# Kernel tuning notes

Hardware: AMD Instinct MI355X
Metric: run time of the kernel (lower is better)

Reference implementation:

```python
import jax, jax.numpy as jnp
import numpy as np

DT = 1.0
TOL = 2e-4
MAX_FK = 0.1


def _lap(x):
    # 5-point Laplacian with periodic boundary (roll-based), x: [B,1,H,W]
    return (jnp.roll(x, 1, -1) + jnp.roll(x, -1, -1)
            + jnp.roll(x, 1, -2) + jnp.roll(x, -1, -2) - 4.0 * x)


def _gs_step(u, v, Du, Dv, F, k, dt):
    uvv = u * v * v
    u_next = u + dt * (Du * _lap(u) - uvv + F * (1.0 - u))
    v_next = v + dt * (Dv * _lap(v) + uvv - (F + k) * v)
    return u_next, v_next


def setup_inputs() -> dict:
    key = jax.random.key(0)
    k1, k2 = jax.random.split(key)
    B, H, W = 32, 512, 512
    # physically sensible Gray-Scott init: u near 1, v small
    u = 1.0 - 0.5 * jax.random.uniform(k1, (B, 1, H, W), dtype=jnp.float32)
    v = 0.25 * jax.random.uniform(k2, (B, 1, H, W), dtype=jnp.float32)
    return {
        "u": u,
        "v": v,
        "log_Du": jnp.float32(-2.0),
        "log_Dv": jnp.float32(-2.0),
        "raw_F": jnp.float32(0.0),
        "raw_k": jnp.float32(0.0),
        "max_steps": 64,
        "K": 32,
    }


def reference(u, v, log_Du, log_Dv, raw_F, raw_k, max_steps, K):
    # params_tensor()
    Du = jax.nn.softplus(log_Du)
    Dv = jax.nn.softplus(log_Dv)
    F = MAX_FK * jax.nn.sigmoid(raw_F)
    k = MAX_FK * jax.nn.sigmoid(raw_k)

    B = u.shape[0]
    converged0 = jnp.zeros((B,), dtype=bool)

    # Phase 1: simulate-until-converged (per-sample freeze), expressed as a
    # fixed-length masked scan (no data-dependent shapes). Samples that were
    # already converged at the start of a step keep their state frozen,
    # matching the index_select/scatter semantics of the torch loop.
    def steady_body(carry, _):
        u, v, conv = carry
        u_next, v_next = _gs_step(u, v, Du, Dv, F, k, DT)
        du = jnp.max(jnp.abs(u_next - u), axis=(1, 2, 3))
        dv = jnp.max(jnp.abs(v_next - v), axis=(1, 2, 3))
        newly = jnp.maximum(du, dv) < TOL
        m = conv[:, None, None, None]
        u2 = jnp.where(m, u, u_next)
        v2 = jnp.where(m, v, v_next)
        return (u2, v2, conv | newly), None

    (u, v, converged), _ = jax.lax.scan(
        steady_body, (u, v, converged0), None, length=max_steps)

    # Phase 2: K differentiable steps (trunc BPTT segment), no masking
    def bptt_body(carry, _):
        u, v = carry
        return _gs_step(u, v, Du, Dv, F, k, DT), None

    (u, v), _ = jax.lax.scan(bptt_body, (u, v), None, length=K)
    return (u, v)
```

## Files before the change

kernel.cpp:

```cpp
#include <hip/hip_runtime.h>

#define HH 512
#define WW 512
#define BB 32
#define NIMG (HH * WW)
#define NT (BB * NIMG)
#define TOLF 0.0002f
#define TR 16
#define TI (TR + 2)
#define NTB (HH / TR)

__device__ __forceinline__ void gs_math(
    const float4& cu, const float4& uu, const float4& ud, float ul, float ur,
    const float4& cv, const float4& vu, const float4& vd, float vl, float vr,
    float Du, float Dv, float F, float Fk, float4& un, float4& vn)
{
    float4 lu, lv;
    lu.x = ul   + cu.y + uu.x + ud.x - 4.f * cu.x;
    lu.y = cu.x + cu.z + uu.y + ud.y - 4.f * cu.y;
    lu.z = cu.y + cu.w + uu.z + ud.z - 4.f * cu.z;
    lu.w = cu.z + ur   + uu.w + ud.w - 4.f * cu.w;
    lv.x = vl   + cv.y + vu.x + vd.x - 4.f * cv.x;
    lv.y = cv.x + cv.z + vu.y + vd.y - 4.f * cv.y;
    lv.z = cv.y + cv.w + vu.z + vd.z - 4.f * cv.z;
    lv.w = cv.z + vr   + vu.w + vd.w - 4.f * cv.w;
    float uvv;
    uvv  = cu.x * cv.x * cv.x;
    un.x = cu.x + (Du * lu.x - uvv + F * (1.f - cu.x));
    vn.x = cv.x + (Dv * lv.x + uvv - Fk * cv.x);
    uvv  = cu.y * cv.y * cv.y;
    un.y = cu.y + (Du * lu.y - uvv + F * (1.f - cu.y));
    vn.y = cv.y + (Dv * lv.y + uvv - Fk * cv.y);
    uvv  = cu.z * cv.z * cv.z;
    un.z = cu.z + (Du * lu.z - uvv + F * (1.f - cu.z));
    vn.z = cv.z + (Dv * lv.z + uvv - Fk * cv.z);
    uvv  = cu.w * cv.w * cv.w;
    un.w = cu.w + (Du * lu.w - uvv + F * (1.f - cu.w));
    vn.w = cv.w + (Dv * lv.w + uvv - Fk * cv.w);
}

__device__ __forceinline__ void load_row(const float* __restrict__ s,
                                         int base, int baseUp, int baseDn, int c0,
                                         float4& c, float4& up, float4& dn, float& l, float& r)
{
    c  = *(const float4*)(s + base   + c0);
    up = *(const float4*)(s + baseUp + c0);
    dn = *(const float4*)(s + baseDn + c0);
    l  = s[base + ((c0 - 1) & (WW - 1))];
    r  = s[base + ((c0 + 4) & (WW - 1))];
}

__device__ __forceinline__ float dmax8(const float4& un, const float4& cu,
                                       const float4& vn, const float4& cv)
{
    return fmaxf(
        fmaxf(fmaxf(fabsf(un.x - cu.x), fabsf(un.y - cu.y)),
              fmaxf(fabsf(un.z - cu.z), fabsf(un.w - cu.w))),
        fmaxf(fmaxf(fabsf(vn.x - cv.x), fabsf(vn.y - cv.y)),
              fmaxf(fabsf(vn.z - cv.z), fabsf(vn.w - cv.w))));
}

__launch_bounds__(256, 2)
__global__ void gs_pair(const float* __restrict__ fsU, const float* __restrict__ fsV,
                        float* wsU, float* wsV, float* outU, float* outV,
                        const float* __restrict__ consts,
                        const int* __restrict__ conv, const int* __restrict__ par,
                        float* __restrict__ pmaxA, float* __restrict__ pmaxB,
                        int tpar, int steady)
{
    __shared__ float iu[TI][WW];
    __shared__ float iv[TI][WW];
    __shared__ float s1[4], s2[4];

    const int b = blockIdx.y;
    if (steady && conv[b]) return;
    const int p = par[b] ^ tpar;
    const float* __restrict__ su = p ? outU : wsU;
    const float* __restrict__ sv = p ? outV : wsV;
    float* __restrict__ dU = p ? wsU : outU;
    float* __restrict__ dV = p ? wsV : outV;
    if (fsU) { su = fsU; sv = fsV; }

    const float Du = consts[0], Dv = consts[1], F = consts[2], Fk = consts[3];

    const int t  = threadIdx.x;
    const int c0 = (t & 127) * 4;
    const int rw = t >> 7;
    const int r0 = blockIdx.x * TR;

    float dm1 = 0.f;
    #pragma unroll
    for (int i = 0; i < TI; i += 2) {
        const int li = i + rw;
        const int h  = (r0 - 1 + li) & (HH - 1);
        const int hm = (h - 1) & (HH - 1);
        const int hp = (h + 1) & (HH - 1);
        const int base   = b * NIMG + h  * WW;
        const int baseUp = b * NIMG + hm * WW;
        const int baseDn = b * NIMG + hp * WW;
        float4 cu, uu, ud, cv, vu, vd; float ul, ur, vl, vr;
        load_row(su, base, baseUp, baseDn, c0, cu, uu, ud, ul, ur);
        load_row(sv, base, baseUp, baseDn, c0, cv, vu, vd, vl, vr);
        float4 un, vn;
        gs_math(cu, uu, ud, ul, ur, cv, vu, vd, vl, vr, Du, Dv, F, Fk, un, vn);
        *(float4*)(&iu[li][c0]) = un;
        *(float4*)(&iv[li][c0]) = vn;
        if (steady) dm1 = fmaxf(dm1, dmax8(un, cu, vn, cv));
    }
    __syncthreads();

    float dm2 = 0.f;
    #pragma unroll
    for (int i = 0; i < TR; i += 2) {
        const int li = 1 + i + rw;
        const int h  = r0 + i + rw;
        float4 cu = *(const float4*)(&iu[li][c0]);
        float4 uu = *(const float4*)(&iu[li - 1][c0]);
        float4 ud = *(const float4*)(&iu[li + 1][c0]);
        const float ul = iu[li][(c0 - 1) & (WW - 1)];
        const float ur = iu[li][(c0 + 4) & (WW - 1)];
        float4 cv = *(const float4*)(&iv[li][c0]);
        float4 vu = *(const float4*)(&iv[li - 1][c0]);
        float4 vd = *(const float4*)(&iv[li + 1][c0]);
        const float vl = iv[li][(c0 - 1) & (WW - 1)];
        const float vr = iv[li][(c0 + 4) & (WW - 1)];
        float4 un, vn;
        gs_math(cu, uu, ud, ul, ur, cv, vu, vd, vl, vr, Du, Dv, F, Fk, un, vn);
        *(float4*)(dU + b * NIMG + h * WW + c0) = un;
        *(float4*)(dV + b * NIMG + h * WW + c0) = vn;
        if (steady) dm2 = fmaxf(dm2, dmax8(un, cu, vn, cv));
    }

    if (steady) {
        #pragma unroll
        for (int off = 1; off < 64; off <<= 1) {
            dm1 = fmaxf(dm1, __shfl_xor(dm1, off));
            dm2 = fmaxf(dm2, __shfl_xor(dm2, off));
        }
        const int wid = t >> 6;
        if ((t & 63) == 0) { s1[wid] = dm1; s2[wid] = dm2; }
        __syncthreads();
        if (t == 0) {
            pmaxA[b * NTB + blockIdx.x] = fmaxf(fmaxf(s1[0], s1[1]), fmaxf(s1[2], s1[3]));
            pmaxB[b * NTB + blockIdx.x] = fmaxf(fmaxf(s2[0], s2[1]), fmaxf(s2[2], s2[3]));
        }
    }
}

__launch_bounds__(256, 2)
__global__ void gs_upd(const float* __restrict__ fsU, const float* __restrict__ fsV,
                       float* wsU, float* wsV, float* outU, float* outV,
                       const float* __restrict__ consts,
                       const int* __restrict__ convO, const int* __restrict__ parO,
                       int* convN, int* parN,
                       const float* __restrict__ pmaxA, const float* __restrict__ pmaxB)
{
    __shared__ float sAB[2];
    const int b = blockIdx.y;
    const int t = threadIdx.x;
    if (convO[b]) {
        if (blockIdx.x == 0 && t == 0) { convN[b] = 1; parN[b] = parO[b]; }
        return;
    }
    if (t < 64) {
        float a = (t < NTB) ? pmaxA[b * NTB + t] : 0.f;
        float c = (t < NTB) ? pmaxB[b * NTB + t] : 0.f;
        #pragma unroll
        for (int off = 1; off < 32; off <<= 1) {
            a = fmaxf(a, __shfl_xor(a, off));
            c = fmaxf(c, __shfl_xor(c, off));
        }
        if (t == 0) { sAB[0] = a; sAB[1] = c; }
    }
    __syncthreads();
    const float d1 = sAB[0], d2 = sAB[1];
    const int pO = parO[b];
    if (blockIdx.x == 0 && t == 0) {
        parN[b]  = pO ^ 1;
        convN[b] = (d1 < TOLF) || (d2 < TOLF);
    }
    if (d1 < TOLF) {
        const float* __restrict__ su = pO ? outU : wsU;
        const float* __restrict__ sv = pO ? outV : wsV;
        float* __restrict__ dU = pO ? wsU : outU;
        float* __restrict__ dV = pO ? wsV : outV;
        if (fsU) { su = fsU; sv = fsV; }
        const float Du = consts[0], Dv = consts[1], F = consts[2], Fk = consts[3];
        const int c0 = (t & 127) * 4;
        const int rw = t >> 7;
        const int r0 = blockIdx.x * TR;
        for (int i = 0; i < TR; i += 2) {
            const int h  = r0 + i + rw;
            const int hm = (h - 1) & (HH - 1);
            const int hp = (h + 1) & (HH - 1);
            const int base   = b * NIMG + h  * WW;
            const int baseUp = b * NIMG + hm * WW;
            const int baseDn = b * NIMG + hp * WW;
            float4 cu, uu, ud, cv, vu, vd; float ul, ur, vl, vr;
            load_row(su, base, baseUp, baseDn, c0, cu, uu, ud, ul, ur);
            load_row(sv, base, baseUp, baseDn, c0, cv, vu, vd, vl, vr);
            float4 un, vn;
            gs_math(cu, uu, ud, ul, ur, cv, vu, vd, vl, vr, Du, Dv, F, Fk, un, vn);
            *(float4*)(dU + base + c0) = un;
            *(float4*)(dV + base + c0) = vn;
        }
    }
}

__global__ void gs_init(const float* lDu, const float* lDv, const float* rF, const float* rk,
                        float* consts, int* conv0, int* par0)
{
    const int t = threadIdx.x;
    if (t == 0) {
        const float a = lDu[0], c = lDv[0];
        const float Du = (a > 0.f) ? a + log1pf(expf(-a)) : log1pf(expf(a));
        const float Dv = (c > 0.f) ? c + log1pf(expf(-c)) : log1pf(expf(c));
        const float F  = 0.1f / (1.f + expf(-rF[0]));
        const float kk = 0.1f / (1.f + expf(-rk[0]));
        consts[0] = Du; consts[1] = Dv; consts[2] = F; consts[3] = F + kk;
    }
    if (t < BB) { conv0[t] = 0; par0[t] = 0; }
}

__launch_bounds__(256)
__global__ void gs_final(const float* __restrict__ wsU, const float* __restrict__ wsV,
                         float* outU, float* outV, const int* __restrict__ par)
{
    const int b = blockIdx.y;
    if (par[b] != 0) return;
    const int off = b * NIMG + (blockIdx.x * 256 + threadIdx.x) * 4;
    *(float4*)(outU + off) = *(const float4*)(wsU + off);
    *(float4*)(outV + off) = *(const float4*)(wsV + off);
}

extern "C" void kernel_launch(void* const* d_in, const int* in_sizes, int n_in,
                              void* d_out, int out_size, void* d_ws, size_t ws_size,
                              hipStream_t stream)
{
    const float* in_u = (const float*)d_in[0];
    const float* in_v = (const float*)d_in[1];
    const float* lDu  = (const float*)d_in[2];
    const float* lDv  = (const float*)d_in[3];
    const float* rF   = (const float*)d_in[4];
    const float* rk   = (const float*)d_in[5];
    const int NPAIR_STEADY = 32;
    const int NPAIR_BPTT   = 16;

    float* wsU = (float*)d_ws;
    float* wsV = wsU + NT;
    float* aux = wsV + NT;
    float* consts = aux;
    int* conv0 = (int*)(aux + 4);
    int* par0  = conv0 + BB;
    int* conv1 = par0 + BB;
    int* par1  = conv1 + BB;
    float* pmaxA = (float*)(par1 + BB);
    float* pmaxB = pmaxA + BB * NTB;

    float* outU = (float*)d_out;
    float* outV = outU + NT;

    gs_init<<<1, 64, 0, stream>>>(lDu, lDv, rF, rk, consts, conv0, par0);

    const dim3 grid(NTB, BB);
    for (int s = 0; s < NPAIR_STEADY; ++s) {
        int* cO = (s & 1) ? conv1 : conv0;
        int* pO = (s & 1) ? par1  : par0;
        int* cN = (s & 1) ? conv0 : conv1;
        int* pN = (s & 1) ? par0  : par1;
        const float* fU = (s == 0) ? in_u : nullptr;
        const float* fV = (s == 0) ? in_v : nullptr;
        gs_pair<<<grid, 256, 0, stream>>>(fU, fV, wsU, wsV, outU, outV, consts,
                                          cO, pO, pmaxA, pmaxB, 0, 1);
        gs_upd<<<grid, 256, 0, stream>>>(fU, fV, wsU, wsV, outU, outV, consts,
                                         cO, pO, cN, pN, pmaxA, pmaxB);
    }
    for (int j = 0; j < NPAIR_BPTT; ++j) {
        gs_pair<<<grid, 256, 0, stream>>>(nullptr, nullptr, wsU, wsV, outU, outV, consts,
                                          conv0, par0, pmaxA, pmaxB, j & 1, 0);
    }
    gs_final<<<dim3(NIMG / 1024, BB), 256, 0, stream>>>(wsU, wsV, outU, outV, par0);
}
```

Measured before the change: 1.595 ms.

## Fuse four Gray-Scott steps per kernel with rolling shared-memory ring pipeline

Replaces the two-step temporal-blocked kernel with a four-step kernel that streams 32-row strips through a chain of 5-row shared-memory ring buffers. Each intermediate step is computed from the previous stage's ring, and per-step max-deltas are recorded for the convergence check. The aim is to halve global memory traffic and kernel launches per simulated step. Samples that converge partway through a quad are recomputed from the quad's input by rollback kernels (rollA does two steps, rollB one), which adds launches and extra work on convergence. The strip grid is smaller (16x32 blocks) and the kernel uses more shared memory, which may lower occupancy.

```diff
diff --git a/kernel.cpp b/kernel.cpp
--- a/kernel.cpp
+++ b/kernel.cpp
@@ -6,9 +6,11 @@
 #define NIMG (HH * WW)
 #define NT (BB * NIMG)
 #define TOLF 0.0002f
-#define TR 16
-#define TI (TR + 2)
-#define NTB (HH / TR)
+#define HS 32
+#define NSTRIP (HH / HS)
+#define TRP 16
+#define TIP (TRP + 2)
+#define NTBP (HH / TRP)
 
 __device__ __forceinline__ void gs_math(
     const float4& cu, const float4& uu, const float4& ud, float ul, float ur,
@@ -39,17 +41,6 @@
     vn.w = cv.w + (Dv * lv.w + uvv - Fk * cv.w);
 }
 
-__device__ __forceinline__ void load_row(const float* __restrict__ s,
-                                         int base, int baseUp, int baseDn, int c0,
-                                         float4& c, float4& up, float4& dn, float& l, float& r)
-{
-    c  = *(const float4*)(s + base   + c0);
-    up = *(const float4*)(s + baseUp + c0);
-    dn = *(const float4*)(s + baseDn + c0);
-    l  = s[base + ((c0 - 1) & (WW - 1))];
-    r  = s[base + ((c0 + 4) & (WW - 1))];
-}
-
 __device__ __forceinline__ float dmax8(const float4& un, const float4& cu,
                                        const float4& vn, const float4& cv)
 {
@@ -60,17 +51,41 @@
               fmaxf(fabsf(vn.z - cv.z), fabsf(vn.w - cv.w))));
 }
 
-__launch_bounds__(256, 2)
-__global__ void gs_pair(const float* __restrict__ fsU, const float* __restrict__ fsV,
-                        float* wsU, float* wsV, float* outU, float* outV,
-                        const float* __restrict__ consts,
-                        const int* __restrict__ conv, const int* __restrict__ par,
-                        float* __restrict__ pmaxA, float* __restrict__ pmaxB,
-                        int tpar, int steady)
-{
-    __shared__ float iu[TI][WW];
-    __shared__ float iv[TI][WW];
-    __shared__ float s1[4], s2[4];
+__device__ __forceinline__ int s5(int r) { int m = r % 5; return m < 0 ? m + 5 : m; }
+
+__device__ __forceinline__ void produce_ring(
+    const float (* __restrict__ Su)[WW], const float (* __restrict__ Sv)[WW],
+    float (* __restrict__ Tu)[WW], float (* __restrict__ Tv)[WW],
+    int r, int c0, float Du, float Dv, float F, float Fk, float& dm, bool acc)
+{
+    const int sm = s5(r - 1), s0 = s5(r), sp = s5(r + 1);
+    const int cl = (c0 - 4) & (WW - 1), cr = (c0 + 4) & (WW - 1);
+    const float4 cu = *(const float4*)&Su[s0][c0];
+    const float4 uu = *(const float4*)&Su[sm][c0];
+    const float4 ud = *(const float4*)&Su[sp][c0];
+    const float  ul = ((const float4*)&Su[s0][cl])->w;
+    const float  ur = ((const float4*)&Su[s0][cr])->x;
+    const float4 cv = *(const float4*)&Sv[s0][c0];
+    const float4 vu = *(const float4*)&Sv[sm][c0];
+    const float4 vd = *(const float4*)&Sv[sp][c0];
+    const float  vl = ((const float4*)&Sv[s0][cl])->w;
+    const float  vr = ((const float4*)&Sv[s0][cr])->x;
+    float4 un, vn;
+    gs_math(cu, uu, ud, ul, ur, cv, vu, vd, vl, vr, Du, Dv, F, Fk, un, vn);
+    *(float4*)&Tu[s0][c0] = un;
+    *(float4*)&Tv[s0][c0] = vn;
+    if (acc) dm = fmaxf(dm, dmax8(un, cu, vn, cv));
+}
+
+__global__ __launch_bounds__(256)
+void gs_quad(const float* __restrict__ fsU, const float* __restrict__ fsV,
+             float* wsU, float* wsV, float* outU, float* outV,
+             const float* __restrict__ consts,
+             const int* __restrict__ conv, const int* __restrict__ par,
+             float* __restrict__ pmax, int tpar, int steady)
+{
+    __shared__ float Iu[5][WW], Iv[5][WW], Au[5][WW], Av[5][WW],
+                     Bu[5][WW], Bv[5][WW], Cu[5][WW], Cv[5][WW];
 
     const int b = blockIdx.y;
     if (steady && conv[b]) return;
@@ -82,15 +97,170 @@
     if (fsU) { su = fsU; sv = fsV; }
 
     const float Du = consts[0], Dv = consts[1], F = consts[2], Fk = consts[3];
-
     const int t  = threadIdx.x;
+    const int rw = t >> 7;
     const int c0 = (t & 127) * 4;
-    const int rw = t >> 7;
-    const int r0 = blockIdx.x * TR;
-
-    float dm1 = 0.f;
+    const int R0 = blockIdx.x * HS;
+    const size_t ib = (size_t)b * NIMG;
+
+    float d1 = 0.f, d2 = 0.f, d3 = 0.f, d4 = 0.f;
+
+    float4 pu, pv;
+    {   const int g = (R0 - 4 + rw) & (HH - 1);
+        pu = *(const float4*)(su + ib + (size_t)g * WW + c0);
+        pv = *(const float4*)(sv + ib + (size_t)g * WW + c0);
+    }
+
+    for (int i = 0; i < 24; ++i) {
+        const int rI = 2*i - 4  + rw;
+        const int rA = 2*i - 6  + rw;
+        const int rB = 2*i - 10 + rw;
+        const int rC = 2*i - 12 + rw;
+        const int rO = 2*i - 16 + rw;
+
+        if (rI <= HS + 3) {
+            const int s = s5(rI);
+            *(float4*)&Iu[s][c0] = pu;
+            *(float4*)&Iv[s][c0] = pv;
+        }
+        if (rB >= -2 && rB <= HS + 1)
+            produce_ring(Au, Av, Bu, Bv, rB, c0, Du, Dv, F, Fk, d2,
+                         steady && rB >= 0 && rB < HS);
+        if (rO >= 0 && rO < HS) {
+            const int sm = s5(rO - 1), s0 = s5(rO), sp = s5(rO + 1);
+            const int cl = (c0 - 4) & (WW - 1), cr = (c0 + 4) & (WW - 1);
+            const float4 cu = *(const float4*)&Cu[s0][c0];
+            const float4 uu = *(const float4*)&Cu[sm][c0];
+            const float4 ud = *(const float4*)&Cu[sp][c0];
+            const float  ul = ((const float4*)&Cu[s0][cl])->w;
+            const float  ur = ((const float4*)&Cu[s0][cr])->x;
+            const float4 cv = *(const float4*)&Cv[s0][c0];
+            const float4 vu = *(const float4*)&Cv[sm][c0];
+            const float4 vd = *(const float4*)&Cv[sp][c0];
+            const float  vl = ((const float4*)&Cv[s0][cl])->w;
+            const float  vr = ((const float4*)&Cv[s0][cr])->x;
+            float4 un, vn;
+            gs_math(cu, uu, ud, ul, ur, cv, vu, vd, vl, vr, Du, Dv, F, Fk, un, vn);
+            *(float4*)(dU + ib + (size_t)(R0 + rO) * WW + c0) = un;
+            *(float4*)(dV + ib + (size_t)(R0 + rO) * WW + c0) = vn;
+            if (steady) d4 = fmaxf(d4, dmax8(un, cu, vn, cv));
+        }
+        __syncthreads();
+
+        {   const int rn = 2*i - 2 + rw;
+            if (rn <= HS + 3) {
+                const int g = (R0 + rn) & (HH - 1);
+                pu = *(const float4*)(su + ib + (size_t)g * WW + c0);
+                pv = *(const float4*)(sv + ib + (size_t)g * WW + c0);
+            }
+        }
+
+        if (rA >= -3 && rA <= HS + 2)
+            produce_ring(Iu, Iv, Au, Av, rA, c0, Du, Dv, F, Fk, d1,
+                         steady && rA >= 0 && rA < HS);
+        if (rC >= -1 && rC <= HS)
+            produce_ring(Bu, Bv, Cu, Cv, rC, c0, Du, Dv, F, Fk, d3,
+                         steady && rC >= 0 && rC < HS);
+        __syncthreads();
+    }
+
+    if (steady) {
+        #pragma unroll
+        for (int off = 1; off < 64; off <<= 1) {
+            d1 = fmaxf(d1, __shfl_xor(d1, off));
+            d2 = fmaxf(d2, __shfl_xor(d2, off));
+            d3 = fmaxf(d3, __shfl_xor(d3, off));
+            d4 = fmaxf(d4, __shfl_xor(d4, off));
+        }
+        const int w = t >> 6;
+        if ((t & 63) == 0) {
+            Iu[0][w * 4 + 0] = d1; Iu[0][w * 4 + 1] = d2;
+            Iu[0][w * 4 + 2] = d3; Iu[0][w * 4 + 3] = d4;
+        }
+        __syncthreads();
+        if (t == 0) {
+            float m0 = 0.f, m1 = 0.f, m2 = 0.f, m3 = 0.f;
+            #pragma unroll
+            for (int w2 = 0; w2 < 4; ++w2) {
+                m0 = fmaxf(m0, Iu[0][w2 * 4 + 0]);
+                m1 = fmaxf(m1, Iu[0][w2 * 4 + 1]);
+                m2 = fmaxf(m2, Iu[0][w2 * 4 + 2]);
+                m3 = fmaxf(m3, Iu[0][w2 * 4 + 3]);
+            }
+            const int idx = b * NSTRIP + blockIdx.x;
+            pmax[0 * BB * NSTRIP + idx] = m0;
+            pmax[1 * BB * NSTRIP + idx] = m1;
+            pmax[2 * BB * NSTRIP + idx] = m2;
+            pmax[3 * BB * NSTRIP + idx] = m3;
+        }
+    }
+}
+
+__global__ void gs_upd(const int* __restrict__ convO, const int* __restrict__ parO,
+                       int* convN, int* parN, int* rbJ,
+                       const float* __restrict__ pmax)
+{
+    const int b = blockIdx.x, t = threadIdx.x;
+    if (convO[b]) { if (t == 0) { convN[b] = 1; parN[b] = parO[b]; rbJ[b] = 0; } return; }
+    float v0 = 0.f, v1 = 0.f, v2 = 0.f, v3 = 0.f;
+    if (t < NSTRIP) {
+        const int idx = b * NSTRIP + t;
+        v0 = pmax[0 * BB * NSTRIP + idx];
+        v1 = pmax[1 * BB * NSTRIP + idx];
+        v2 = pmax[2 * BB * NSTRIP + idx];
+        v3 = pmax[3 * BB * NSTRIP + idx];
+    }
     #pragma unroll
-    for (int i = 0; i < TI; i += 2) {
+    for (int off = 1; off < NSTRIP; off <<= 1) {
+        v0 = fmaxf(v0, __shfl_xor(v0, off));
+        v1 = fmaxf(v1, __shfl_xor(v1, off));
+        v2 = fmaxf(v2, __shfl_xor(v2, off));
+        v3 = fmaxf(v3, __shfl_xor(v3, off));
+    }
+    if (t == 0) {
+        int j = 0;
+        if      (v0 < TOLF) j = 1;
+        else if (v1 < TOLF) j = 2;
+        else if (v2 < TOLF) j = 3;
+        else if (v3 < TOLF) j = 4;
+        const int pO = parO[b];
+        convN[b] = (j != 0);
+        parN[b]  = (j == 3) ? pO : (pO ^ 1);
+        rbJ[b]   = (j >= 1 && j <= 3) ? j : 0;
+    }
+}
+
+__device__ __forceinline__ void load_row(const float* __restrict__ s,
+                                         int base, int baseUp, int baseDn, int c0,
+                                         float4& c, float4& up, float4& dn, float& l, float& r)
+{
+    c  = *(const float4*)(s + base   + c0);
+    up = *(const float4*)(s + baseUp + c0);
+    dn = *(const float4*)(s + baseDn + c0);
+    l  = s[base + ((c0 - 1) & (WW - 1))];
+    r  = s[base + ((c0 + 4) & (WW - 1))];
+}
+
+__global__ __launch_bounds__(256)
+void gs_rollA(const float* __restrict__ fsU, const float* __restrict__ fsV,
+              float* wsU, float* wsV, float* outU, float* outV,
+              const float* __restrict__ consts,
+              const int* __restrict__ parO, const int* __restrict__ rbJ)
+{
+    __shared__ float iu[TIP][WW];
+    __shared__ float iv[TIP][WW];
+    const int b = blockIdx.y;
+    if (rbJ[b] < 2) return;
+    const int p = parO[b];
+    const float* __restrict__ su = p ? outU : wsU;
+    const float* __restrict__ sv = p ? outV : wsV;
+    float* __restrict__ dU = p ? wsU : outU;
+    float* __restrict__ dV = p ? wsV : outV;
+    if (fsU) { su = fsU; sv = fsV; }
+    const float Du = consts[0], Dv = consts[1], F = consts[2], Fk = consts[3];
+    const int t = threadIdx.x, c0 = (t & 127) * 4, rw = t >> 7;
+    const int r0 = blockIdx.x * TRP;
+    for (int i = 0; i < TIP; i += 2) {
         const int li = i + rw;
         const int h  = (r0 - 1 + li) & (HH - 1);
         const int hm = (h - 1) & (HH - 1);
@@ -105,13 +275,9 @@
         gs_math(cu, uu, ud, ul, ur, cv, vu, vd, vl, vr, Du, Dv, F, Fk, un, vn);
         *(float4*)(&iu[li][c0]) = un;
         *(float4*)(&iv[li][c0]) = vn;
-        if (steady) dm1 = fmaxf(dm1, dmax8(un, cu, vn, cv));
     }
     __syncthreads();
-
-    float dm2 = 0.f;
-    #pragma unroll
-    for (int i = 0; i < TR; i += 2) {
+    for (int i = 0; i < TRP; i += 2) {
         const int li = 1 + i + rw;
         const int h  = r0 + i + rw;
         float4 cu = *(const float4*)(&iu[li][c0]);
@@ -128,87 +294,44 @@
         gs_math(cu, uu, ud, ul, ur, cv, vu, vd, vl, vr, Du, Dv, F, Fk, un, vn);
         *(float4*)(dU + b * NIMG + h * WW + c0) = un;
         *(float4*)(dV + b * NIMG + h * WW + c0) = vn;
-        if (steady) dm2 = fmaxf(dm2, dmax8(un, cu, vn, cv));
-    }
-
-    if (steady) {
-        #pragma unroll
-        for (int off = 1; off < 64; off <<= 1) {
-            dm1 = fmaxf(dm1, __shfl_xor(dm1, off));
-            dm2 = fmaxf(dm2, __shfl_xor(dm2, off));
-        }
-        const int wid = t >> 6;
-        if ((t & 63) == 0) { s1[wid] = dm1; s2[wid] = dm2; }
-        __syncthreads();
-        if (t == 0) {
-            pmaxA[b * NTB + blockIdx.x] = fmaxf(fmaxf(s1[0], s1[1]), fmaxf(s1[2], s1[3]));
-            pmaxB[b * NTB + blockIdx.x] = fmaxf(fmaxf(s2[0], s2[1]), fmaxf(s2[2], s2[3]));
-        }
-    }
-}
-
-__launch_bounds__(256, 2)
-__global__ void gs_upd(const float* __restrict__ fsU, const float* __restrict__ fsV,
-                       float* wsU, float* wsV, float* outU, float* outV,
-                       const float* __restrict__ consts,
-                       const int* __restrict__ convO, const int* __restrict__ parO,
-                       int* convN, int* parN,
-                       const float* __restrict__ pmaxA, const float* __restrict__ pmaxB)
-{
-    __shared__ float sAB[2];
+    }
+}
+
+__global__ __launch_bounds__(256)
+void gs_rollB(const float* __restrict__ fsU, const float* __restrict__ fsV,
+              float* wsU, float* wsV, float* outU, float* outV,
+              const float* __restrict__ consts,
+              const int* __restrict__ parO, const int* __restrict__ rbJ)
+{
     const int b = blockIdx.y;
-    const int t = threadIdx.x;
-    if (convO[b]) {
-        if (blockIdx.x == 0 && t == 0) { convN[b] = 1; parN[b] = parO[b]; }
-        return;
-    }
-    if (t < 64) {
-        float a = (t < NTB) ? pmaxA[b * NTB + t] : 0.f;
-        float c = (t < NTB) ? pmaxB[b * NTB + t] : 0.f;
-        #pragma unroll
-        for (int off = 1; off < 32; off <<= 1) {
-            a = fmaxf(a, __shfl_xor(a, off));
-            c = fmaxf(c, __shfl_xor(c, off));
-        }
-        if (t == 0) { sAB[0] = a; sAB[1] = c; }
-    }
-    __syncthreads();
-    const float d1 = sAB[0], d2 = sAB[1];
-    const int pO = parO[b];
-    if (blockIdx.x == 0 && t == 0) {
-        parN[b]  = pO ^ 1;
-        convN[b] = (d1 < TOLF) || (d2 < TOLF);
-    }
-    if (d1 < TOLF) {
-        const float* __restrict__ su = pO ? outU : wsU;
-        const float* __restrict__ sv = pO ? outV : wsV;
-        float* __restrict__ dU = pO ? wsU : outU;
-        float* __restrict__ dV = pO ? wsV : outV;
-        if (fsU) { su = fsU; sv = fsV; }
-        const float Du = consts[0], Dv = consts[1], F = consts[2], Fk = consts[3];
-        const int c0 = (t & 127) * 4;
-        const int rw = t >> 7;
-        const int r0 = blockIdx.x * TR;
-        for (int i = 0; i < TR; i += 2) {
-            const int h  = r0 + i + rw;
-            const int hm = (h - 1) & (HH - 1);
-            const int hp = (h + 1) & (HH - 1);
-            const int base   = b * NIMG + h  * WW;
-            const int baseUp = b * NIMG + hm * WW;
-            const int baseDn = b * NIMG + hp * WW;
-            float4 cu, uu, ud, cv, vu, vd; float ul, ur, vl, vr;
-            load_row(su, base, baseUp, baseDn, c0, cu, uu, ud, ul, ur);
-            load_row(sv, base, baseUp, baseDn, c0, cv, vu, vd, vl, vr);
-            float4 un, vn;
-            gs_math(cu, uu, ud, ul, ur, cv, vu, vd, vl, vr, Du, Dv, F, Fk, un, vn);
-            *(float4*)(dU + base + c0) = un;
-            *(float4*)(dV + base + c0) = vn;
-        }
-    }
+    const int j = rbJ[b];
+    if (j != 1 && j != 3) return;
+    const int q = parO[b] ^ (j == 3 ? 1 : 0);
+    const float* __restrict__ su = q ? outU : wsU;
+    const float* __restrict__ sv = q ? outV : wsV;
+    float* __restrict__ dU = q ? wsU : outU;
+    float* __restrict__ dV = q ? wsV : outV;
+    if (j == 1 && fsU) { su = fsU; sv = fsV; }
+    const float Du = consts[0], Dv = consts[1], F = consts[2], Fk = consts[3];
+    const int idx = blockIdx.x * 256 + threadIdx.x;
+    const int h  = idx >> 7;
+    const int c0 = (idx & 127) * 4;
+    const int hm = (h - 1) & (HH - 1);
+    const int hp = (h + 1) & (HH - 1);
+    const int base   = b * NIMG + h  * WW;
+    const int baseUp = b * NIMG + hm * WW;
+    const int baseDn = b * NIMG + hp * WW;
+    float4 cu, uu, ud, cv, vu, vd; float ul, ur, vl, vr;
+    load_row(su, base, baseUp, baseDn, c0, cu, uu, ud, ul, ur);
+    load_row(sv, base, baseUp, baseDn, c0, cv, vu, vd, vl, vr);
+    float4 un, vn;
+    gs_math(cu, uu, ud, ul, ur, cv, vu, vd, vl, vr, Du, Dv, F, Fk, un, vn);
+    *(float4*)(dU + base + c0) = un;
+    *(float4*)(dV + base + c0) = vn;
 }
 
 __global__ void gs_init(const float* lDu, const float* lDv, const float* rF, const float* rk,
-                        float* consts, int* conv0, int* par0)
+                        float* consts, int* conv0, int* par0, int* rbJ)
 {
     const int t = threadIdx.x;
     if (t == 0) {
@@ -219,7 +342,7 @@
         const float kk = 0.1f / (1.f + expf(-rk[0]));
         consts[0] = Du; consts[1] = Dv; consts[2] = F; consts[3] = F + kk;
     }
-    if (t < BB) { conv0[t] = 0; par0[t] = 0; }
+    if (t < BB) { conv0[t] = 0; par0[t] = 0; rbJ[t] = 0; }
 }
 
 __launch_bounds__(256)
@@ -243,8 +366,8 @@
     const float* lDv  = (const float*)d_in[3];
     const float* rF   = (const float*)d_in[4];
     const float* rk   = (const float*)d_in[5];
-    const int NPAIR_STEADY = 32;
-    const int NPAIR_BPTT   = 16;
+    const int NQUAD_STEADY = 16;
+    const int NQUAD_BPTT   = 8;
 
     float* wsU = (float*)d_ws;
     float* wsV = wsU + NT;
@@ -254,30 +377,33 @@
     int* par0  = conv0 + BB;
     int* conv1 = par0 + BB;
     int* par1  = conv1 + BB;
-    float* pmaxA = (float*)(par1 + BB);
-    float* pmaxB = pmaxA + BB * NTB;
+    int* rbJ   = par1 + BB;
+    float* pmax = (float*)(rbJ + BB);
 
     float* outU = (float*)d_out;
     float* outV = outU + NT;
 
-    gs_init<<<1, 64, 0, stream>>>(lDu, lDv, rF, rk, consts, conv0, par0);
-
-    const dim3 grid(NTB, BB);
-    for (int s = 0; s < NPAIR_STEADY; ++s) {
+    gs_init<<<1, 64, 0, stream>>>(lDu, lDv, rF, rk, consts, conv0, par0, rbJ);
+
+    const dim3 gridQ(NSTRIP, BB);
+    for (int s = 0; s < NQUAD_STEADY; ++s) {
         int* cO = (s & 1) ? conv1 : conv0;
         int* pO = (s & 1) ? par1  : par0;
         int* cN = (s & 1) ? conv0 : conv1;
         int* pN = (s & 1) ? par0  : par1;
         const float* fU = (s == 0) ? in_u : nullptr;
         const float* fV = (s == 0) ? in_v : nullptr;
-        gs_pair<<<grid, 256, 0, stream>>>(fU, fV, wsU, wsV, outU, outV, consts,
-                                          cO, pO, pmaxA, pmaxB, 0, 1);
-        gs_upd<<<grid, 256, 0, stream>>>(fU, fV, wsU, wsV, outU, outV, consts,
-                                         cO, pO, cN, pN, pmaxA, pmaxB);
-    }
-    for (int j = 0; j < NPAIR_BPTT; ++j) {
-        gs_pair<<<grid, 256, 0, stream>>>(nullptr, nullptr, wsU, wsV, outU, outV, consts,
-                                          conv0, par0, pmaxA, pmaxB, j & 1, 0);
+        gs_quad<<<gridQ, 256, 0, stream>>>(fU, fV, wsU, wsV, outU, outV, consts,
+                                           cO, pO, pmax, 0, 1);
+        gs_upd<<<BB, 64, 0, stream>>>(cO, pO, cN, pN, rbJ, pmax);
+        gs_rollA<<<dim3(NTBP, BB), 256, 0, stream>>>(fU, fV, wsU, wsV, outU, outV,
+                                                     consts, pO, rbJ);
+        gs_rollB<<<dim3(NIMG / 1024, BB), 256, 0, stream>>>(fU, fV, wsU, wsV, outU, outV,
+                                                            consts, pO, rbJ);
+    }
+    for (int j = 0; j < NQUAD_BPTT; ++j) {
+        gs_quad<<<gridQ, 256, 0, stream>>>(nullptr, nullptr, wsU, wsV, outU, outV, consts,
+                                           conv0, par0, pmax, j & 1, 0);
     }
     gs_final<<<dim3(NIMG / 1024, BB), 256, 0, stream>>>(wsU, wsV, outU, outV, par0);
 }
```

New measurement: 1.288 ms. 1.24x faster.
